# Optimization experiments

Measured on AMD Instinct MI355X. Metric: run time of the kernel, lower is better.

Reference implementation:

```python
import jax, jax.numpy as jnp
import numpy as np

H, DH, DIM = 8, 64, 512
GAMMA, LAMBDA_REG = 0.01, 0.001


def setup_inputs() -> dict:
    key = jax.random.key(0)
    ks = jax.random.split(key, 12)
    Q, N = 4, 1024
    f = lambda k, shape, s=0.02: jax.random.normal(k, shape, dtype=jnp.float32) * s
    return {
        "q": jax.random.normal(ks[0], (Q, N, DIM), dtype=jnp.float32),
        "k": jax.random.normal(ks[1], (Q, N, DIM), dtype=jnp.float32),
        "v": jax.random.normal(ks[2], (Q, N, DIM), dtype=jnp.float32),
        "ln_w": jnp.ones((DIM,), jnp.float32),
        "ln_b": jnp.zeros((DIM,), jnp.float32),
        "W_in": f(ks[3], (DIM, H * DH)),
        "W_out": f(ks[4], (H * DH, DIM)),
        "b_out": jnp.zeros((DIM,), jnp.float32),
        "wp_W1": f(ks[5], (2 * DH, 4 * DH), 0.05),
        "wp_b1": jnp.zeros((4 * DH,), jnp.float32),
        "wp_ln_w": jnp.ones((4 * DH,), jnp.float32),
        "wp_ln_b": jnp.zeros((4 * DH,), jnp.float32),
        "wp_W2": f(ks[6], (4 * DH, 3 * DH), 0.05),
        "wp_b2": jnp.zeros((3 * DH,), jnp.float32),
        "wp_W3": f(ks[7], (3 * DH, DH), 0.05),
        "wp_b3": jnp.zeros((DH,), jnp.float32),
        "wp_W4": f(ks[8], (DH, 3), 0.05),
        "wp_b4": jnp.zeros((3,), jnp.float32),
        "weight_temp": jnp.ones((1,), jnp.float32) * 0.1,
    }


def _layernorm(x, w, b, eps=1e-5):
    mu = x.mean(-1, keepdims=True)
    var = x.var(-1, keepdims=True)  # biased, matches torch LayerNorm
    return (x - mu) / jnp.sqrt(var + eps) * w + b


def reference(q, k, v, ln_w, ln_b, W_in, W_out, b_out,
              wp_W1, wp_b1, wp_ln_w, wp_ln_b, wp_W2, wp_b2,
              wp_W3, wp_b3, wp_W4, wp_b4, weight_temp):
    # input_linear: LN -> Linear(no bias) -> (dropout=identity in eval)
    def proj(t):
        x = _layernorm(t, ln_w, ln_b) @ W_in  # [Q, N, H*DH]
        Qn, Nn = x.shape[0], x.shape[1]
        return x.reshape(Qn, Nn, H, DH).transpose(2, 0, 1, 3)  # h q n d

    fq, fk, fv = proj(q), proj(k), proj(v)
    m = fk.shape[2]

    # --- cosine component (cosine_distance + extra clamp) ---
    raw = jnp.einsum('hqnd,hqmd->hqnm', fq, fk)
    n1 = jnp.linalg.norm(fq, axis=-1)[..., :, None] + 1e-6
    n2 = jnp.linalg.norm(fk, axis=-1)[..., None, :] + 1e-6
    cosine_sim = jnp.clip(raw / (n1 * n2), -0.95, 0.95)

    # --- regularized covariance component ---
    fkc = fk - fk.mean(axis=2, keepdims=True)       # center keys over token dim
    fqc = fq - fq.mean(axis=-1, keepdims=True)      # center queries over feature dim
    cov = jnp.einsum('hqnd,hqmd->hqnm', fqc, fkc) / (DH ** 0.5 + 1e-4)
    cov = jnp.clip((LAMBDA_REG / max(m, 1)) * cov, -50.0, 50.0)

    # --- margin-based variance component (eval: adaptive_gamma = gamma) ---
    fqn = fq / jnp.maximum(jnp.linalg.norm(fq, axis=-1, keepdims=True), 1e-4)
    fkn = fk / jnp.maximum(jnp.linalg.norm(fk, axis=-1, keepdims=True), 1e-4)
    cs = jnp.clip(jnp.einsum('hqnd,hqmd->hqnm', fqn, fkn), -0.95, 0.95)
    margin = jnp.clip(GAMMA - cs, 0.0, 15.0)
    var_comp = jnp.broadcast_to(margin.mean(-1, keepdims=True), cs.shape)

    # --- dynamic per-head weights via MLP predictor ---
    feat = jnp.concatenate([fq.mean(axis=(1, 2)), fk.mean(axis=(1, 2))], axis=-1)  # (h, 2*DH)
    h1 = jax.nn.relu(_layernorm(feat @ wp_W1 + wp_b1, wp_ln_w, wp_ln_b))
    h2 = jax.nn.relu(h1 @ wp_W2 + wp_b2)
    h3 = jax.nn.relu(h2 @ wp_W3 + wp_b3)
    probs = jax.nn.softmax(h3 @ wp_W4 + wp_b4, axis=-1)  # predictor ends in Softmax
    wt = jnp.clip(weight_temp, 0.01, 1.0)
    w = jax.nn.softmax(probs / wt, axis=-1)
    w = jnp.clip(w, 0.01, 0.95)
    w = w / w.sum(-1, keepdims=True)
    cos_w = w[:, 0].reshape(H, 1, 1, 1)
    cov_w = w[:, 1].reshape(H, 1, 1, 1)
    var_w = w[:, 2].reshape(H, 1, 1, 1)

    # --- std-normalized weighted combination (torch.std is unbiased, detached) ---
    sg = jax.lax.stop_gradient
    ustd = lambda x: jnp.std(x, ddof=1)
    dots = (cos_w * (cosine_sim / (sg(ustd(cosine_sim)) + 1e-4))
            + cov_w * (cov / (sg(ustd(cov)) + 1e-4) * 0.3)
            + var_w * (var_comp / (sg(ustd(var_comp)) + 1e-4) * 0.3))

    ds = ustd(dots)  # NOT detached in original
    temp = jnp.where(ds < 1e-5, 0.01, jnp.where(ds < 1e-3, 0.05, 0.2 + ds * 2.0))
    temp = jnp.clip(temp, 0.01, 8.0)

    attn = jax.nn.softmax(dots / temp, axis=-1)
    out = jnp.einsum('hqnm,hqmd->hqnd', attn, fv)
    out = out.transpose(1, 2, 0, 3).reshape(out.shape[1], out.shape[2], H * DH)  # q n (h d)
    return out @ W_out + b_out
```

## Files before the change

### kernel.cpp

```cpp
#include <hip/hip_runtime.h>
#include <math.h>

typedef _Float16 f16;
typedef _Float16 v8h __attribute__((ext_vector_type(8)));
typedef _Float16 v4h __attribute__((ext_vector_type(4)));
typedef float    v4f __attribute__((ext_vector_type(4)));

#define MFMA(a, b, c) __builtin_amdgcn_mfma_f32_16x16x32_f16((a), (b), (c), 0, 0, 0)

#define OFF_LN16    0u
#define OFF_FQ16    4194304u
#define OFF_FK16    5242880u
#define OFF_FVHT    6291456u
#define OFF_WINTH   8388608u
#define OFF_WOUTTH  8650752u
#define OFF_AVH     8912896u
#define OFF_AVL     9961472u
#define OFF_RQ1     11010048u
#define OFF_RQ2     11042816u
#define OFF_MUQ     11075584u
#define OFF_RK1     11108352u
#define OFF_RK2     11141120u
#define OFF_SK      11173888u
#define OFF_VC      11206656u
#define OFF_ROWCOS  11272192u
#define OFF_ROWCOV  11337728u
#define OFF_NUACC   11403264u
#define OFF_PB      11405312u
#define OFF_HS      11411456u
#define OFF_RP      11411520u
#define OFF_FEAT    11411712u
#define OFF_WV      11412736u
#define OFF_SCAL    11412760u

__device__ __forceinline__ float clampf(float x, float lo, float hi) {
    return fminf(fmaxf(x, lo), hi);
}

__global__ void k_zero(float* feat, float* nuacck) {
    int i = blockIdx.x * 256 + threadIdx.x;
    if (i < 1024) feat[i] = 0.0f;
    if (i < 2048) nuacck[i] = 0.0f;
}

__global__ __launch_bounds__(256) void k_wprep(const float* __restrict__ Win,
        const float* __restrict__ Wout, f16* __restrict__ WinTh,
        f16* __restrict__ WoutTh) {
    __shared__ float lds[64][68];
    const float* W = blockIdx.z ? Wout : Win;
    f16* Th = blockIdx.z ? WoutTh : WinTh;
    int k0 = blockIdx.y * 64, c0 = blockIdx.x * 64;
    int t = threadIdx.x;
    #pragma unroll
    for (int p = 0; p < 4; ++p) {
        int flat = p * 1024 + t * 4;
        int r = flat >> 6, c = flat & 63;
        *(float4*)&lds[r][c] = *(const float4*)&W[(size_t)(k0 + r) * 512 + c0 + c];
    }
    __syncthreads();
    int c = t >> 2, kk = (t & 3) * 16;
    #pragma unroll
    for (int half = 0; half < 2; ++half) {
        v8h h8;
        #pragma unroll
        for (int ii = 0; ii < 8; ++ii)
            h8[ii] = (f16)lds[kk + half * 8 + ii][c];
        *(v8h*)&Th[(size_t)(c0 + c) * 512 + k0 + kk + half * 8] = h8;
    }
}

__global__ __launch_bounds__(256) void k_ln16(const float* __restrict__ q,
        const float* __restrict__ kk, const float* __restrict__ v,
        const float* __restrict__ lnw, const float* __restrict__ lnb,
        f16* __restrict__ ln16) {
    int t = threadIdx.x, wid = t >> 6, lane = t & 63;
    int token = blockIdx.x * 4 + wid;
    int inp = token >> 12, lt = token & 4095;
    const float* xp = (inp == 0) ? q : ((inp == 1) ? kk : v);
    const float4* xr = (const float4*)(xp + (size_t)lt * 512);
    float4 a = xr[lane], b = xr[lane + 64];
    float s = a.x + a.y + a.z + a.w + b.x + b.y + b.z + b.w;
    float s2 = a.x*a.x + a.y*a.y + a.z*a.z + a.w*a.w
             + b.x*b.x + b.y*b.y + b.z*b.z + b.w*b.w;
    for (int o = 32; o > 0; o >>= 1) { s += __shfl_down(s, o); s2 += __shfl_down(s2, o); }
    float m_ = __shfl(s, 0) * (1.0f / 512.0f);
    float var = __shfl(s2, 0) * (1.0f / 512.0f) - m_ * m_;
    var = fmaxf(var, 0.0f);
    float rs = rsqrtf(var + 1e-5f);
    const float4* w4 = (const float4*)lnw;
    const float4* b4 = (const float4*)lnb;
    float4 wa = w4[lane], wb = w4[lane + 64], ba = b4[lane], bb = b4[lane + 64];
    f16* orow = ln16 + (size_t)token * 512;
    v4h ha, hb;
    ha[0] = (f16)((a.x - m_) * rs * wa.x + ba.x);
    ha[1] = (f16)((a.y - m_) * rs * wa.y + ba.y);
    ha[2] = (f16)((a.z - m_) * rs * wa.z + ba.z);
    ha[3] = (f16)((a.w - m_) * rs * wa.w + ba.w);
    hb[0] = (f16)((b.x - m_) * rs * wb.x + bb.x);
    hb[1] = (f16)((b.y - m_) * rs * wb.y + bb.y);
    hb[2] = (f16)((b.z - m_) * rs * wb.z + bb.z);
    hb[3] = (f16)((b.w - m_) * rs * wb.w + bb.w);
    *(v4h*)&orow[lane * 4] = ha;
    *(v4h*)&orow[lane * 4 + 256] = hb;
}

template<int MODE>
__device__ __forceinline__ void proj_body(const f16* __restrict__ A16,
        const f16* __restrict__ BTh,
        f16* __restrict__ fout16, f16* __restrict__ fhT,
        float* __restrict__ oA, float* __restrict__ oB, float* __restrict__ oC,
        float* __restrict__ feat, float* __restrict__ nuacck) {
    int t = threadIdx.x, l = t & 63, w = t >> 6;
    int wr = w >> 1, wc = w & 1;
    int col0 = blockIdx.x * 128 + wc * 64;
    int tok0 = blockIdx.y * 128 + wr * 64;
    int lr = l & 15, kg = (l >> 4) * 8;
    int rg4 = (l >> 4) * 4;
    v4f acc[4][4] = {};
    for (int ks = 0; ks < 512; ks += 32) {
        v8h a[4], b[4];
        #pragma unroll
        for (int i = 0; i < 4; ++i)
            a[i] = *(const v8h*)&A16[(size_t)(tok0 + i * 16 + lr) * 512 + ks + kg];
        #pragma unroll
        for (int j = 0; j < 4; ++j)
            b[j] = *(const v8h*)&BTh[(size_t)(col0 + j * 16 + lr) * 512 + ks + kg];
        #pragma unroll
        for (int i = 0; i < 4; ++i)
            #pragma unroll
            for (int j = 0; j < 4; ++j)
                acc[i][j] = MFMA(a[i], b[j], acc[i][j]);
    }
    int h = col0 >> 6;
    #pragma unroll
    for (int i = 0; i < 4; ++i)
        #pragma unroll
        for (int j = 0; j < 4; ++j)
            #pragma unroll
            for (int r = 0; r < 4; ++r) {
                int token = tok0 + i * 16 + rg4 + r;
                int d = j * 16 + lr;
                int qi = token >> 10, n = token & 1023;
                float val = acc[i][j][r];
                if constexpr (MODE != 2) {
                    fout16[((size_t)((h << 2) + qi) * 1024 + n) * 64 + d] = (f16)val;
                } else {
                    fhT[((size_t)((h << 2) + qi) * 64 + d) * 1024 + n] = (f16)val;
                }
            }
    if constexpr (MODE != 2) {
        #pragma unroll
        for (int i = 0; i < 4; ++i)
            #pragma unroll
            for (int r = 0; r < 4; ++r) {
                float s = 0.f, s2 = 0.f;
                #pragma unroll
                for (int j = 0; j < 4; ++j) { float v = acc[i][j][r]; s += v; s2 += v * v; }
                #pragma unroll
                for (int mk = 1; mk <= 8; mk <<= 1) {
                    s += __shfl_xor(s, mk); s2 += __shfl_xor(s2, mk);
                }
                if (lr == 0) {
                    int token = tok0 + i * 16 + rg4 + r;
                    int qi = token >> 10, n = token & 1023;
                    int row = ((h << 2) + qi) * 1024 + n;
                    float nv = sqrtf(s2);
                    oA[row] = 1.0f / (nv + 1e-6f);
                    oB[row] = 1.0f / fmaxf(nv, 1e-4f);
                    oC[row] = (MODE == 0) ? s * (1.0f / 64.0f) : s;
                }
            }
        float cs[4];
        #pragma unroll
        for (int j = 0; j < 4; ++j) {
            float c = 0.f;
            #pragma unroll
            for (int i = 0; i < 4; ++i)
                #pragma unroll
                for (int r = 0; r < 4; ++r) c += acc[i][j][r];
            c += __shfl_xor(c, 16); c += __shfl_xor(c, 32);
            cs[j] = c;
        }
        if (l < 16) {
            #pragma unroll
            for (int j = 0; j < 4; ++j)
                atomicAdd(&feat[h * 128 + (MODE == 1 ? 64 : 0) + j * 16 + l],
                          cs[j] * (1.0f / 4096.0f));
            if constexpr (MODE == 1) {
                int qi = tok0 >> 10;
                #pragma unroll
                for (int j = 0; j < 4; ++j)
                    atomicAdd(&nuacck[((h << 2) + qi) * 64 + j * 16 + l], cs[j]);
            }
        }
    }
}

__global__ __launch_bounds__(256) void k_proj_all(const f16* __restrict__ ln16,
        const f16* __restrict__ BTh,
        f16* __restrict__ fq16, f16* __restrict__ fk16,
        f16* __restrict__ fvhT,
        float* __restrict__ rq1, float* __restrict__ rq2, float* __restrict__ muq,
        float* __restrict__ rk1, float* __restrict__ rk2, float* __restrict__ sk,
        float* __restrict__ feat, float* __restrict__ nuacck) {
    int mode = blockIdx.z;
    if (mode == 0)
        proj_body<0>(ln16, BTh, fq16, nullptr, rq1, rq2, muq, feat, nullptr);
    else if (mode == 1)
        proj_body<1>(ln16 + 2097152u, BTh, fk16, nullptr, rk1, rk2, sk, feat, nuacck);
    else
        proj_body<2>(ln16 + 4194304u, BTh, nullptr, fvhT,
                     nullptr, nullptr, nullptr, nullptr, nullptr);
}

__global__ __launch_bounds__(256) void k_mlp(const float* __restrict__ feat,
        const float* __restrict__ W1, const float* __restrict__ b1,
        const float* __restrict__ lw, const float* __restrict__ lb,
        const float* __restrict__ W2, const float* __restrict__ b2,
        const float* __restrict__ W3, const float* __restrict__ b3,
        const float* __restrict__ W4, const float* __restrict__ b4,
        const float* __restrict__ wtemp, float* wv) {
    __shared__ float h1[256], h2[192], h3[64], red[8];
    int t = threadIdx.x;
    int h = blockIdx.x;
    float p = 0.0f;
    for (int i = 0; i < 128; ++i) p += feat[h * 128 + i] * W1[i * 256 + t];
    p += b1[t];
    float s = p, s2 = p * p;
    for (int o = 32; o > 0; o >>= 1) { s += __shfl_down(s, o); s2 += __shfl_down(s2, o); }
    if ((t & 63) == 0) { red[t >> 6] = s; red[4 + (t >> 6)] = s2; }
    __syncthreads();
    float S = red[0] + red[1] + red[2] + red[3];
    float S2 = red[4] + red[5] + red[6] + red[7];
    float mu = S / 256.0f;
    float var = S2 / 256.0f - mu * mu; if (var < 0.0f) var = 0.0f;
    float xh = (p - mu) * rsqrtf(var + 1e-5f) * lw[t] + lb[t];
    h1[t] = fmaxf(xh, 0.0f);
    __syncthreads();
    if (t < 192) {
        float a = 0.0f;
        for (int i = 0; i < 256; ++i) a += h1[i] * W2[i * 192 + t];
        h2[t] = fmaxf(a + b2[t], 0.0f);
    }
    __syncthreads();
    if (t < 64) {
        float a = 0.0f;
        for (int i = 0; i < 192; ++i) a += h2[i] * W3[i * 64 + t];
        h3[t] = fmaxf(a + b3[t], 0.0f);
    }
    __syncthreads();
    if (t == 0) {
        float lg[3];
        for (int j = 0; j < 3; ++j) {
            float a = 0.0f;
            for (int i = 0; i < 64; ++i) a += h3[i] * W4[i * 3 + j];
            lg[j] = a + b4[j];
        }
        float mx = fmaxf(lg[0], fmaxf(lg[1], lg[2]));
        float e0 = expf(lg[0] - mx), e1 = expf(lg[1] - mx), e2 = expf(lg[2] - mx);
        float se = e0 + e1 + e2;
        float pr0 = e0 / se, pr1 = e1 / se, pr2 = e2 / se;
        float wt = wtemp[0]; wt = fminf(fmaxf(wt, 0.01f), 1.0f);
        float q0 = pr0 / wt, q1 = pr1 / wt, q2 = pr2 / wt;
        float m2 = fmaxf(q0, fmaxf(q1, q2));
        float f0 = expf(q0 - m2), f1 = expf(q1 - m2), f2 = expf(q2 - m2);
        float sf = f0 + f1 + f2; f0 /= sf; f1 /= sf; f2 /= sf;
        f0 = fminf(fmaxf(f0, 0.01f), 0.95f);
        f1 = fminf(fmaxf(f1, 0.01f), 0.95f);
        f2 = fminf(fmaxf(f2, 0.01f), 0.95f);
        float sw = f0 + f1 + f2;
        wv[h * 3 + 0] = f0 / sw; wv[h * 3 + 1] = f1 / sw; wv[h * 3 + 2] = f2 / sw;
    }
}

#define PASS_PREAMBLE_AB                                                       \
    int hq = blockIdx.z;                                                       \
    int half = blockIdx.y;                                                     \
    int m0base = half * 512;                                                   \
    int t = threadIdx.x, l = t & 63, w = t >> 6;                               \
    int lr = l & 15, kg = (l >> 4) * 8, rg4 = (l >> 4) * 4;                    \
    int nb = blockIdx.x * 64 + w * 16;                                         \
    const f16* Q = fq16 + (size_t)hq * 65536;                                  \
    const f16* K = fk16 + (size_t)hq * 65536;                                  \
    v8h aq0 = *(const v8h*)&Q[(size_t)(nb + lr) * 64 + kg];                    \
    v8h aq1 = *(const v8h*)&Q[(size_t)(nb + lr) * 64 + 32 + kg];               \
    const float inv1024 = 1.0f / 1024.0f;                                      \
    float uvp = nuacck[hq * 64 + l] * inv1024;                                 \
    _Pragma("unroll")                                                          \
    for (int o = 32; o > 0; o >>= 1) uvp += __shfl_xor(uvp, o);                \
    float uv = uvp;                                                            \
    float tp = 0.f;                                                            \
    _Pragma("unroll")                                                          \
    for (int e = 0; e < 8; ++e)                                                \
        tp += (float)aq0[e] * nuacck[hq * 64 + kg + e]                         \
            + (float)aq1[e] * nuacck[hq * 64 + 32 + kg + e];                   \
    tp *= inv1024;                                                             \
    tp += __shfl_xor(tp, 16);                                                  \
    tp += __shfl_xor(tp, 32);                                                  \
    float muv[4], tv[4];                                                       \
    _Pragma("unroll")                                                          \
    for (int r = 0; r < 4; ++r) {                                              \
        muv[r] = muq[hq * 1024 + nb + rg4 + r];                                \
        tv[r] = __shfl(tp, rg4 + r);                                           \
    }                                                                          \
    const float Acs = (0.001f / 1024.0f) / 8.0001f;                            \
    float Pr[4], Gr[4];                                                        \
    _Pragma("unroll")                                                          \
    for (int r = 0; r < 4; ++r) {                                              \
        Gr[r] = Acs * muv[r];                                                  \
        Pr[r] = Acs * fmaf(muv[r], uv, -tv[r]);                                \
    }

#define LOAD_KTILE(m0a)                                                        \
    v8h b0[4], b1[4];                                                          \
    _Pragma("unroll")                                                          \
    for (int j = 0; j < 4; ++j) {                                              \
        b0[j] = *(const v8h*)&K[(size_t)((m0a) + j * 16 + lr) * 64 + kg];      \
        b1[j] = *(const v8h*)&K[(size_t)((m0a) + j * 16 + lr) * 64 + 32 + kg]; \
    }

__global__ __launch_bounds__(256) void k_passA(const f16* __restrict__ fq16,
        const f16* __restrict__ fk16, const float* __restrict__ rq1,
        const float* __restrict__ rq2, const float* __restrict__ muq,
        const float* __restrict__ rk1, const float* __restrict__ rk2,
        const float* __restrict__ sk, const float* __restrict__ nuacck,
        float* __restrict__ vcrow, float* __restrict__ rowcos,
        float* __restrict__ rowcov, float* __restrict__ pb) {
    __shared__ float rk1s[512], rk2s[512], sks[512];
    PASS_PREAMBLE_AB
    {
        int i2 = t * 2;
        *(float2*)&rk1s[i2] = *(const float2*)&rk1[hq * 1024 + m0base + i2];
        *(float2*)&rk2s[i2] = *(const float2*)&rk2[hq * 1024 + m0base + i2];
        *(float2*)&sks[i2]  = *(const float2*)&sk[hq * 1024 + m0base + i2];
    }
    __syncthreads();
    float rq1v[4], rq2v[4];
    #pragma unroll
    for (int r = 0; r < 4; ++r) {
        rq1v[r] = rq1[hq * 1024 + nb + rg4 + r];
        rq2v[r] = rq2[hq * 1024 + nb + rg4 + r];
    }
    float scos = 0, s2cos = 0, scov = 0, s2cov = 0, sccov = 0;
    float mp[4] = {}, rcs[4] = {}, rcv[4] = {};
    #pragma unroll 2
    for (int m0 = 0; m0 < 512; m0 += 64) {
        LOAD_KTILE(m0base + m0)
        float rk1v[4], rk2v[4], skv[4];
        #pragma unroll
        for (int j = 0; j < 4; ++j) {
            int cg = m0 + j * 16 + lr;
            rk1v[j] = rk1s[cg]; rk2v[j] = rk2s[cg]; skv[j] = sks[cg];
        }
        v4f acc[4] = {};
        #pragma unroll
        for (int j = 0; j < 4; ++j) {
            acc[j] = MFMA(aq0, b0[j], acc[j]);
            acc[j] = MFMA(aq1, b1[j], acc[j]);
        }
        #pragma unroll
        for (int j = 0; j < 4; ++j)
            #pragma unroll
            for (int r = 0; r < 4; ++r) {
                float rv = acc[j][r];
                float cosv = clampf(rv * rq1v[r] * rk1v[j], -0.95f, 0.95f);
                float x2 = rv * rq2v[r] * rk2v[j];
                float marg = fmaxf(0.01f - fmaxf(x2, -0.95f), 0.0f);
                float cov = fmaf(-Gr[r], skv[j], fmaf(Acs, rv, Pr[r]));
                scos += cosv; s2cos = fmaf(cosv, cosv, s2cos);
                scov += cov;  s2cov = fmaf(cov, cov, s2cov);
                sccov = fmaf(cosv, cov, sccov);
                mp[r] += marg; rcs[r] += cosv; rcv[r] += cov;
            }
    }
    #pragma unroll
    for (int r = 0; r < 4; ++r) {
        float m_ = mp[r], c_ = rcs[r], v_ = rcv[r];
        #pragma unroll
        for (int mk = 1; mk <= 8; mk <<= 1) {
            m_ += __shfl_xor(m_, mk);
            c_ += __shfl_xor(c_, mk);
            v_ += __shfl_xor(v_, mk);
        }
        if (lr == 0) {
            int row = hq * 1024 + nb + rg4 + r;
            vcrow[half * 32768 + row] = m_ * inv1024;
            rowcos[half * 32768 + row] = c_;
            rowcov[half * 32768 + row] = v_;
        }
    }
    for (int o = 32; o > 0; o >>= 1) {
        scos += __shfl_down(scos, o); s2cos += __shfl_down(s2cos, o);
        scov += __shfl_down(scov, o); s2cov += __shfl_down(s2cov, o);
        sccov += __shfl_down(sccov, o);
    }
    __shared__ float bs[4][5];
    if (l == 0) { bs[w][0] = scos; bs[w][1] = s2cos; bs[w][2] = scov;
                  bs[w][3] = s2cov; bs[w][4] = sccov; }
    __syncthreads();
    if (t == 0) {
        int bid = (hq * 2 + half) * 16 + blockIdx.x;
        #pragma unroll
        for (int s = 0; s < 5; ++s)
            pb[bid * 6 + s] = bs[0][s] + bs[1][s] + bs[2][s] + bs[3][s];
    }
}

__global__ __launch_bounds__(256) void k_fin1(const float* __restrict__ pb,
        const float* __restrict__ vcrow, float* __restrict__ hs,
        float* __restrict__ scal) {
    __shared__ float hsl[40];
    int t = threadIdx.x;
    int hd = t >> 5, idx = t & 31;
    double a0 = 0, a1 = 0, a2 = 0, a3 = 0, a4 = 0;
    for (int i = idx; i < 128; i += 32) {
        const float* p = &pb[(hd * 128 + i) * 6];
        a0 += p[0]; a1 += p[1]; a2 += p[2]; a3 += p[3]; a4 += p[4];
    }
    for (int m = 1; m <= 16; m <<= 1) {
        a0 += __shfl_xor(a0, m); a1 += __shfl_xor(a1, m); a2 += __shfl_xor(a2, m);
        a3 += __shfl_xor(a3, m); a4 += __shfl_xor(a4, m);
    }
    if (idx == 0) {
        hsl[hd * 5 + 0] = (float)a0; hsl[hd * 5 + 1] = (float)a1;
        hsl[hd * 5 + 2] = (float)a2; hsl[hd * 5 + 3] = (float)a3;
        hsl[hd * 5 + 4] = (float)a4;
        hs[hd * 5 + 0] = (float)a0; hs[hd * 5 + 1] = (float)a1;
        hs[hd * 5 + 2] = (float)a2; hs[hd * 5 + 3] = (float)a3;
        hs[hd * 5 + 4] = (float)a4;
    }
    double s4 = 0, s5 = 0;
    for (int i = t; i < 32768; i += 256) {
        double rm = (double)(vcrow[i] + vcrow[32768 + i]);
        s4 += rm; s5 += rm * rm;
    }
    for (int o = 32; o > 0; o >>= 1) { s4 += __shfl_down(s4, o); s5 += __shfl_down(s5, o); }
    __shared__ double red[2][4];
    int wid = t >> 6, lane = t & 63;
    if (lane == 0) { red[0][wid] = s4; red[1][wid] = s5; }
    __syncthreads();
    if (t == 0) {
        double S4 = red[0][0] + red[0][1] + red[0][2] + red[0][3];
        double S5 = red[1][0] + red[1][1] + red[1][2] + red[1][3];
        double S0 = 0, S1 = 0, S2 = 0, S3 = 0;
        for (int h2 = 0; h2 < 8; ++h2) {
            S0 += hsl[h2 * 5 + 0]; S1 += hsl[h2 * 5 + 1];
            S2 += hsl[h2 * 5 + 2]; S3 += hsl[h2 * 5 + 3];
        }
        const double cnt = 33554432.0;
        scal[0] = (float)sqrt(fmax(0.0, (S1 - S0 * S0 / cnt) / (cnt - 1.0)));
        scal[1] = (float)sqrt(fmax(0.0, (S3 - S2 * S2 / cnt) / (cnt - 1.0)));
        double V4 = S4 * 1024.0, V5 = S5 * 1024.0;
        scal[2] = (float)sqrt(fmax(0.0, (V5 - V4 * V4 / cnt) / (cnt - 1.0)));
    }
}

__global__ __launch_bounds__(256) void k_finrow(const float* __restrict__ vcrow,
        const float* __restrict__ rowcos, const float* __restrict__ rowcov,
        const float* __restrict__ wv, const float* __restrict__ scal,
        float* __restrict__ rp) {
    int t = threadIdx.x;
    float s1 = scal[0] + 1e-4f, s2v = scal[1] + 1e-4f, s3 = scal[2] + 1e-4f;
    float p1 = 0, p2 = 0, p3 = 0;
    #pragma unroll
    for (int i = 0; i < 2; ++i) {
        int row = blockIdx.x * 512 + i * 256 + t;
        int h = row >> 12;
        float fc1 = wv[h * 3] / s1;
        float fc2 = wv[h * 3 + 1] * 0.3f / s2v;
        float c3 = wv[h * 3 + 2] * 0.3f / s3;
        float a = (vcrow[row] + vcrow[32768 + row]) * c3;
        float b = fc1 * (rowcos[row] + rowcos[32768 + row])
                + fc2 * (rowcov[row] + rowcov[32768 + row]);
        p1 += a; p2 = fmaf(a, a, p2); p3 = fmaf(a, b, p3);
    }
    for (int o = 32; o > 0; o >>= 1) {
        p1 += __shfl_down(p1, o); p2 += __shfl_down(p2, o); p3 += __shfl_down(p3, o);
    }
    __shared__ float red[3][4];
    int wid = t >> 6, lane = t & 63;
    if (lane == 0) { red[0][wid] = p1; red[1][wid] = p2; red[2][wid] = p3; }
    __syncthreads();
    if (t == 0) {
        rp[blockIdx.x * 3 + 0] = red[0][0] + red[0][1] + red[0][2] + red[0][3];
        rp[blockIdx.x * 3 + 1] = red[1][0] + red[1][1] + red[1][2] + red[1][3];
        rp[blockIdx.x * 3 + 2] = red[2][0] + red[2][1] + red[2][2] + red[2][3];
    }
}

__global__ __launch_bounds__(64) void k_fin2(const float* __restrict__ rp,
        const float* __restrict__ hs, const float* __restrict__ wv,
        float* __restrict__ scal) {
    int t = threadIdx.x;
    double p1 = rp[t * 3 + 0], p2 = rp[t * 3 + 1], p3 = rp[t * 3 + 2];
    for (int o = 32; o > 0; o >>= 1) {
        p1 += __shfl_down(p1, o); p2 += __shfl_down(p2, o); p3 += __shfl_down(p3, o);
    }
    if (t == 0) {
        double s1 = (double)scal[0] + 1e-4, s2v = (double)scal[1] + 1e-4;
        double sdd = 1024.0 * p1;
        double sdd2 = 2.0 * p3 + 1024.0 * p2;
        for (int h = 0; h < 8; ++h) {
            double fc1 = (double)wv[h * 3] / s1;
            double fc2 = (double)wv[h * 3 + 1] * 0.3 / s2v;
            sdd += fc1 * hs[h * 5 + 0] + fc2 * hs[h * 5 + 2];
            sdd2 += fc1 * fc1 * hs[h * 5 + 1] + fc2 * fc2 * hs[h * 5 + 3]
                  + 2.0 * fc1 * fc2 * hs[h * 5 + 4];
        }
        const double cnt = 33554432.0;
        double ds = sqrt(fmax(0.0, (sdd2 - sdd * sdd / cnt) / (cnt - 1.0)));
        float temp = (ds < 1e-5) ? 0.01f : ((ds < 1e-3) ? 0.05f : (0.2f + (float)ds * 2.0f));
        temp = fminf(fmaxf(temp, 0.01f), 8.0f);
        scal[3] = temp;
    }
}

#define TILE_STEP(PBASE, MK)                                                   \
    {                                                                          \
        int mk = (MK);                                                         \
        v8h b0[4], b1[4];                                                      \
        _Pragma("unroll")                                                      \
        for (int j = 0; j < 4; ++j) {                                          \
            b0[j] = *(const v8h*)&K[(size_t)(mk + j * 16 + lr) * 64 + kg];     \
            b1[j] = *(const v8h*)&K[(size_t)(mk + j * 16 + lr) * 64 + 32 + kg];\
        }                                                                      \
        float rk1v[4], skv[4];                                                 \
        _Pragma("unroll")                                                      \
        for (int j = 0; j < 4; ++j) {                                          \
            int cg = mk + j * 16 + lr;                                         \
            rk1v[j] = rk1s[cg]; skv[j] = sks[cg];                              \
        }                                                                      \
        v4f acc[4] = {};                                                       \
        _Pragma("unroll")                                                      \
        for (int j = 0; j < 4; ++j) {                                          \
            acc[j] = MFMA(aq0, b0[j], acc[j]);                                 \
            acc[j] = MFMA(aq1, b1[j], acc[j]);                                 \
        }                                                                      \
        float dd[4][4];                                                        \
        float tmax[4] = { -1e30f, -1e30f, -1e30f, -1e30f };                    \
        _Pragma("unroll")                                                      \
        for (int j = 0; j < 4; ++j)                                            \
            _Pragma("unroll")                                                  \
            for (int r = 0; r < 4; ++r) {                                      \
                float rv = acc[j][r];                                          \
                float cosv = clampf(rv * rq1v[r] * rk1v[j], -0.95f, 0.95f);    \
                float cov = fmaf(-Gcr[r], skv[j], fmaf(Acs, rv, Pcr[r]));      \
                float d2 = fmaf(fc2, cov, fmaf(fc1, cosv, addc[r]));           \
                dd[j][r] = d2;                                                 \
                tmax[r] = fmaxf(tmax[r], d2);                                  \
            }                                                                  \
        v4f fv;                                                                \
        _Pragma("unroll")                                                      \
        for (int r = 0; r < 4; ++r) {                                          \
            float tm = tmax[r];                                                \
            tm = fmaxf(tm, __shfl_xor(tm, 1));                                 \
            tm = fmaxf(tm, __shfl_xor(tm, 2));                                 \
            tm = fmaxf(tm, __shfl_xor(tm, 4));                                 \
            tm = fmaxf(tm, __shfl_xor(tm, 8));                                 \
            float mnew = fmaxf(mrun[r], tm);                                   \
            float fr_ = __expf((mrun[r] - mnew) * invt);                       \
            mrun[r] = mnew;                                                    \
            rsacc[r] *= fr_;                                                   \
            fv[r] = fr_;                                                       \
        }                                                                      \
        _Pragma("unroll")                                                      \
        for (int j = 0; j < 4; ++j) accpv[j] *= fv;                            \
        _Pragma("unroll")                                                      \
        for (int j = 0; j < 4; ++j)                                            \
            _Pragma("unroll")                                                  \
            for (int r = 0; r < 4; ++r) {                                      \
                float pe = __expf((dd[j][r] - mrun[r]) * invt);                \
                f16 p16 = (f16)pe;                                             \
                rsacc[r] += (float)p16;                                        \
                (PBASE)[(w * 16 + rg4 + r) * 72 + j * 16 + lr] = p16;          \
            }                                                                  \
        v8h pa0 = *(const v8h*)&(PBASE)[(w * 16 + lr) * 72 + kg];              \
        v8h pa1 = *(const v8h*)&(PBASE)[(w * 16 + lr) * 72 + 32 + kg];         \
        _Pragma("unroll")                                                      \
        for (int j = 0; j < 4; ++j) {                                          \
            size_t vb = ((size_t)hq * 64 + j * 16 + lr) * 1024 + mk;           \
            v8h vh0 = *(const v8h*)&fvhT[vb + kg];                             \
            v8h vh1 = *(const v8h*)&fvhT[vb + 32 + kg];                        \
            accpv[j] = MFMA(pa0, vh0, accpv[j]);                               \
            accpv[j] = MFMA(pa1, vh1, accpv[j]);                               \
        }                                                                      \
    }

__global__ __launch_bounds__(512) void k_passC(const f16* __restrict__ fq16,
        const f16* __restrict__ fk16, const float* __restrict__ rq1,
        const float* __restrict__ muq, const float* __restrict__ rk1,
        const float* __restrict__ sk, const float* __restrict__ nuacck,
        const float* __restrict__ vcrow, const float* __restrict__ wv,
        const float* __restrict__ scal,
        const f16* __restrict__ fvhT,
        f16* __restrict__ avh, f16* __restrict__ avl) {
    __shared__ __align__(16) char arena[36864];
    __shared__ float rk1s[1024], sks[1024];
    f16* Pa = (f16*)arena;
    f16* Pb = (f16*)(arena + 18432);
    int hq = blockIdx.y;
    int t = threadIdx.x, l = t & 63, w = t >> 6;
    int rg = w & 3, kh = w >> 2;
    int lr = l & 15, kg = (l >> 4) * 8, rg4 = (l >> 4) * 4;
    int nb = blockIdx.x * 64 + rg * 16;
    int m0base = kh * 512;
    const f16* Q = fq16 + (size_t)hq * 65536;
    const f16* K = fk16 + (size_t)hq * 65536;
    {
        int i2 = t * 2;
        *(float2*)&rk1s[i2] = *(const float2*)&rk1[hq * 1024 + i2];
        *(float2*)&sks[i2]  = *(const float2*)&sk[hq * 1024 + i2];
    }
    __syncthreads();
    v8h aq0 = *(const v8h*)&Q[(size_t)(nb + lr) * 64 + kg];
    v8h aq1 = *(const v8h*)&Q[(size_t)(nb + lr) * 64 + 32 + kg];
    const float inv1024 = 1.0f / 1024.0f;
    float uvp = nuacck[hq * 64 + l] * inv1024;
    #pragma unroll
    for (int o = 32; o > 0; o >>= 1) uvp += __shfl_xor(uvp, o);
    float uv = uvp;
    float tpv = 0.f;
    #pragma unroll
    for (int e = 0; e < 8; ++e)
        tpv += (float)aq0[e] * nuacck[hq * 64 + kg + e]
             + (float)aq1[e] * nuacck[hq * 64 + 32 + kg + e];
    tpv *= inv1024;
    tpv += __shfl_xor(tpv, 16);
    tpv += __shfl_xor(tpv, 32);
    float muv[4], tv[4];
    #pragma unroll
    for (int r = 0; r < 4; ++r) {
        muv[r] = muq[hq * 1024 + nb + rg4 + r];
        tv[r] = __shfl(tpv, rg4 + r);
    }
    const float Acs = (0.001f / 1024.0f) / 8.0001f;
    float Pcr[4], Gcr[4];
    #pragma unroll
    for (int r = 0; r < 4; ++r) {
        Gcr[r] = Acs * muv[r];
        Pcr[r] = Acs * fmaf(muv[r], uv, -tv[r]);
    }
    int h = hq >> 2;
    float s1 = scal[0] + 1e-4f, s2v = scal[1] + 1e-4f, s3 = scal[2] + 1e-4f;
    float fc1 = wv[h * 3] / s1;
    float fc2 = wv[h * 3 + 1] * 0.3f / s2v;
    float c3 = wv[h * 3 + 2] * 0.3f / s3;
    float invt = 1.0f / scal[3];
    float rq1v[4], addc[4];
    #pragma unroll
    for (int r = 0; r < 4; ++r) {
        int row = hq * 1024 + nb + rg4 + r;
        rq1v[r] = rq1[row];
        addc[r] = (vcrow[row] + vcrow[32768 + row]) * c3;
    }
    v4f accpv[4] = {};
    float rsacc[4] = {};
    float mrun[4] = { -1e30f, -1e30f, -1e30f, -1e30f };
    for (int it = 0; it < 4; ++it) {
        TILE_STEP(Pa, m0base + it * 128)
        TILE_STEP(Pb, m0base + it * 128 + 64)
    }
    __syncthreads();
    #pragma unroll
    for (int r = 0; r < 4; ++r) {
        float s = rsacc[r];
        s += __shfl_xor(s, 1); s += __shfl_xor(s, 2);
        s += __shfl_xor(s, 4); s += __shfl_xor(s, 8);
        rsacc[r] = s;
    }
    float* cbacc = (float*)arena;
    float* cbrs  = (float*)(arena + 16384);
    float* cbm   = (float*)(arena + 20480);
    if (kh == 1) {
        #pragma unroll
        for (int j = 0; j < 4; ++j)
            #pragma unroll
            for (int r = 0; r < 4; ++r)
                cbacc[(rg * 16 + j * 4 + r) * 64 + l] = accpv[j][r];
        #pragma unroll
        for (int r = 0; r < 4; ++r) cbrs[(rg * 4 + r) * 64 + l] = rsacc[r];
        if (lr == 0) {
            #pragma unroll
            for (int r = 0; r < 4; ++r) cbm[rg * 16 + rg4 + r] = mrun[r];
        }
    }
    __syncthreads();
    if (kh == 0) {
        v4f f0v, f1v;
        float rinv[4];
        #pragma unroll
        for (int r = 0; r < 4; ++r) {
            float m1 = cbm[rg * 16 + rg4 + r];
            float mf = fmaxf(mrun[r], m1);
            float f0 = __expf((mrun[r] - mf) * invt);
            float f1 = __expf((m1 - mf) * invt);
            f0v[r] = f0; f1v[r] = f1;
            float rst = rsacc[r] * f0 + cbrs[(rg * 4 + r) * 64 + l] * f1;
            rinv[r] = 1.0f / rst;
        }
        #pragma unroll
        for (int j = 0; j < 4; ++j)
            #pragma unroll
            for (int r = 0; r < 4; ++r) {
                float val = (accpv[j][r] * f0v[r]
                           + cbacc[(rg * 16 + j * 4 + r) * 64 + l] * f1v[r]) * rinv[r];
                size_t idx = ((size_t)(hq * 1024 + nb + rg4 + r)) * 64 + j * 16 + lr;
                f16 hi = (f16)val;
                avh[idx] = hi;
                avl[idx] = (f16)(val - (float)hi);
            }
    }
}

__global__ __launch_bounds__(256) void k_out_mfma(const f16* __restrict__ avh,
        const f16* __restrict__ avl,
        const f16* __restrict__ WoutTh,
        const float* __restrict__ bout, float* __restrict__ out) {
    __shared__ float red[2][4][4][4][64];
    int t = threadIdx.x, l = t & 63, w = t >> 6;
    int wc = w & 1, kh = w >> 1;
    int col0 = blockIdx.x * 128 + wc * 64;
    int tok0 = blockIdx.y * 64;
    int qi = tok0 >> 10, nb = tok0 & 1023;
    int lr = l & 15, kg = (l >> 4) * 8;
    v4f acc[4][4] = {};
    for (int ks8 = 0; ks8 < 8; ++ks8) {
        int ks = kh * 256 + ks8 * 32;
        int f = ks + kg;
        int h = f >> 6, d = f & 63;
        size_t hb = (size_t)((h << 2) + qi) * 1024;
        v8h ah[4], al4[4], bh[4];
        #pragma unroll
        for (int i = 0; i < 4; ++i) {
            int n = nb + i * 16 + lr;
            ah[i]  = *(const v8h*)&avh[(hb + n) * 64 + d];
            al4[i] = *(const v8h*)&avl[(hb + n) * 64 + d];
        }
        #pragma unroll
        for (int j = 0; j < 4; ++j)
            bh[j] = *(const v8h*)&WoutTh[(size_t)(col0 + j * 16 + lr) * 512 + ks + kg];
        #pragma unroll
        for (int i = 0; i < 4; ++i)
            #pragma unroll
            for (int j = 0; j < 4; ++j) {
                acc[i][j] = MFMA(ah[i], bh[j], acc[i][j]);
                acc[i][j] = MFMA(al4[i], bh[j], acc[i][j]);
            }
    }
    if (kh == 0) {
        #pragma unroll
        for (int i = 0; i < 4; ++i)
            #pragma unroll
            for (int j = 0; j < 4; ++j)
                #pragma unroll
                for (int r = 0; r < 4; ++r)
                    red[wc][i][j][r][l] = acc[i][j][r];
    }
    __syncthreads();
    if (kh == 1) {
        #pragma unroll
        for (int i = 0; i < 4; ++i)
            #pragma unroll
            for (int j = 0; j < 4; ++j) {
                int col = col0 + j * 16 + lr;
                float bo = bout[col];
                #pragma unroll
                for (int r = 0; r < 4; ++r) {
                    float val = acc[i][j][r] + red[wc][i][j][r][l] + bo;
                    int token = tok0 + i * 16 + (l >> 4) * 4 + r;
                    out[(size_t)token * 512 + col] = val;
                }
            }
    }
}

extern "C" void kernel_launch(void* const* d_in, const int* in_sizes, int n_in,
                              void* d_out, int out_size, void* d_ws, size_t ws_size,
                              hipStream_t stream) {
    const float* q     = (const float*)d_in[0];
    const float* k     = (const float*)d_in[1];
    const float* v     = (const float*)d_in[2];
    const float* ln_w  = (const float*)d_in[3];
    const float* ln_b  = (const float*)d_in[4];
    const float* W_in  = (const float*)d_in[5];
    const float* W_out = (const float*)d_in[6];
    const float* b_out = (const float*)d_in[7];
    const float* wp_W1 = (const float*)d_in[8];
    const float* wp_b1 = (const float*)d_in[9];
    const float* wp_lw = (const float*)d_in[10];
    const float* wp_lb = (const float*)d_in[11];
    const float* wp_W2 = (const float*)d_in[12];
    const float* wp_b2 = (const float*)d_in[13];
    const float* wp_W3 = (const float*)d_in[14];
    const float* wp_b3 = (const float*)d_in[15];
    const float* wp_W4 = (const float*)d_in[16];
    const float* wp_b4 = (const float*)d_in[17];
    const float* wtemp = (const float*)d_in[18];

    float* ws = (float*)d_ws;
    f16* ln16     = (f16*)(ws + OFF_LN16);
    f16* fq16     = (f16*)(ws + OFF_FQ16);
    f16* fk16     = (f16*)(ws + OFF_FK16);
    f16* fvhT     = (f16*)(ws + OFF_FVHT);
    f16* WinTh    = (f16*)(ws + OFF_WINTH);
    f16* WoutTh   = (f16*)(ws + OFF_WOUTTH);
    f16* avh      = (f16*)(ws + OFF_AVH);
    f16* avl      = (f16*)(ws + OFF_AVL);
    float* rq1    = ws + OFF_RQ1;
    float* rq2    = ws + OFF_RQ2;
    float* muq    = ws + OFF_MUQ;
    float* rk1    = ws + OFF_RK1;
    float* rk2    = ws + OFF_RK2;
    float* sk     = ws + OFF_SK;
    float* vcrow  = ws + OFF_VC;
    float* rowcos = ws + OFF_ROWCOS;
    float* rowcov = ws + OFF_ROWCOV;
    float* nuacck = ws + OFF_NUACC;
    float* pb     = ws + OFF_PB;
    float* hs     = ws + OFF_HS;
    float* rp     = ws + OFF_RP;
    float* feat   = ws + OFF_FEAT;
    float* wv     = ws + OFF_WV;
    float* scal   = ws + OFF_SCAL;

    k_zero<<<8, 256, 0, stream>>>(feat, nuacck);
    k_wprep<<<dim3(8, 8, 2), 256, 0, stream>>>(W_in, W_out, WinTh, WoutTh);
    k_ln16<<<3072, 256, 0, stream>>>(q, k, v, ln_w, ln_b, ln16);
    k_proj_all<<<dim3(4, 32, 3), 256, 0, stream>>>(ln16, WinTh,
            fq16, fk16, fvhT, rq1, rq2, muq, rk1, rk2, sk, feat, nuacck);
    k_mlp<<<8, 256, 0, stream>>>(feat, wp_W1, wp_b1, wp_lw, wp_lb,
                                 wp_W2, wp_b2, wp_W3, wp_b3, wp_W4, wp_b4,
                                 wtemp, wv);
    k_passA<<<dim3(16, 2, 32), 256, 0, stream>>>(fq16, fk16, rq1, rq2, muq, rk1, rk2,
                                                 sk, nuacck, vcrow, rowcos, rowcov, pb);
    k_fin1<<<1, 256, 0, stream>>>(pb, vcrow, hs, scal);
    k_finrow<<<64, 256, 0, stream>>>(vcrow, rowcos, rowcov, wv, scal, rp);
    k_fin2<<<1, 64, 0, stream>>>(rp, hs, wv, scal);
    k_passC<<<dim3(16, 32), 512, 0, stream>>>(fq16, fk16, rq1, muq, rk1, sk, nuacck,
                                              vcrow, wv, scal, fvhT, avh, avl);
    k_out_mfma<<<dim3(4, 64), 256, 0, stream>>>(avh, avl, WoutTh, b_out,
                                                (float*)d_out);
}
```

Baseline: 262.1 us.

## Precompute per-row softmax max bound in passA to drop online rescaling in passC

passA now also records, for each row, the maximum clamped cosine and covariance values, reduced across lanes and written for both halves. passC combines these with its positive weights into an upper bound on each row's logit maximum. Each tile then exponentiates directly against that fixed bound. This removes the per-tile max reduction, the running-max exp rescaling of the accumulators, and the final cross-wave max merge. The trade-off is a few extra writes and reads, and a bound that can be looser than the true max, which risks underflow or precision loss in the f16 probabilities if the cosine and covariance maxima land on different columns.

```diff
diff --git a/kernel.cpp b/kernel.cpp
--- a/kernel.cpp
+++ b/kernel.cpp
@@ -32,6 +32,8 @@
 #define OFF_FEAT    11411712u
 #define OFF_WV      11412736u
 #define OFF_SCAL    11412760u
+#define OFF_MAXC    11412768u
+#define OFF_MAXV    11478304u
 
 __device__ __forceinline__ float clampf(float x, float lo, float hi) {
     return fminf(fmaxf(x, lo), hi);
@@ -325,7 +327,8 @@
         const float* __restrict__ rk1, const float* __restrict__ rk2,
         const float* __restrict__ sk, const float* __restrict__ nuacck,
         float* __restrict__ vcrow, float* __restrict__ rowcos,
-        float* __restrict__ rowcov, float* __restrict__ pb) {
+        float* __restrict__ rowcov, float* __restrict__ maxc,
+        float* __restrict__ maxv, float* __restrict__ pb) {
     __shared__ float rk1s[512], rk2s[512], sks[512];
     PASS_PREAMBLE_AB
     {
@@ -343,6 +346,8 @@
     }
     float scos = 0, s2cos = 0, scov = 0, s2cov = 0, sccov = 0;
     float mp[4] = {}, rcs[4] = {}, rcv[4] = {};
+    float mcs[4] = { -1e30f, -1e30f, -1e30f, -1e30f };
+    float mcv[4] = { -1e30f, -1e30f, -1e30f, -1e30f };
     #pragma unroll 2
     for (int m0 = 0; m0 < 512; m0 += 64) {
         LOAD_KTILE(m0base + m0)
@@ -371,22 +376,29 @@
                 scov += cov;  s2cov = fmaf(cov, cov, s2cov);
                 sccov = fmaf(cosv, cov, sccov);
                 mp[r] += marg; rcs[r] += cosv; rcv[r] += cov;
+                mcs[r] = fmaxf(mcs[r], cosv);
+                mcv[r] = fmaxf(mcv[r], cov);
             }
     }
     #pragma unroll
     for (int r = 0; r < 4; ++r) {
         float m_ = mp[r], c_ = rcs[r], v_ = rcv[r];
+        float xc = mcs[r], xv = mcv[r];
         #pragma unroll
         for (int mk = 1; mk <= 8; mk <<= 1) {
             m_ += __shfl_xor(m_, mk);
             c_ += __shfl_xor(c_, mk);
             v_ += __shfl_xor(v_, mk);
+            xc = fmaxf(xc, __shfl_xor(xc, mk));
+            xv = fmaxf(xv, __shfl_xor(xv, mk));
         }
         if (lr == 0) {
             int row = hq * 1024 + nb + rg4 + r;
             vcrow[half * 32768 + row] = m_ * inv1024;
             rowcos[half * 32768 + row] = c_;
             rowcov[half * 32768 + row] = v_;
+            maxc[half * 32768 + row] = xc;
+            maxv[half * 32768 + row] = xv;
         }
     }
     for (int o = 32; o > 0; o >>= 1) {
@@ -536,8 +548,6 @@
             acc[j] = MFMA(aq0, b0[j], acc[j]);                                 \
             acc[j] = MFMA(aq1, b1[j], acc[j]);                                 \
         }                                                                      \
-        float dd[4][4];                                                        \
-        float tmax[4] = { -1e30f, -1e30f, -1e30f, -1e30f };                    \
         _Pragma("unroll")                                                      \
         for (int j = 0; j < 4; ++j)                                            \
             _Pragma("unroll")                                                  \
@@ -546,30 +556,7 @@
                 float cosv = clampf(rv * rq1v[r] * rk1v[j], -0.95f, 0.95f);    \
                 float cov = fmaf(-Gcr[r], skv[j], fmaf(Acs, rv, Pcr[r]));      \
                 float d2 = fmaf(fc2, cov, fmaf(fc1, cosv, addc[r]));           \
-                dd[j][r] = d2;                                                 \
-                tmax[r] = fmaxf(tmax[r], d2);                                  \
-            }                                                                  \
-        v4f fv;                                                                \
-        _Pragma("unroll")                                                      \
-        for (int r = 0; r < 4; ++r) {                                          \
-            float tm = tmax[r];                                                \
-            tm = fmaxf(tm, __shfl_xor(tm, 1));                                 \
-            tm = fmaxf(tm, __shfl_xor(tm, 2));                                 \
-            tm = fmaxf(tm, __shfl_xor(tm, 4));                                 \
-            tm = fmaxf(tm, __shfl_xor(tm, 8));                                 \
-            float mnew = fmaxf(mrun[r], tm);                                   \
-            float fr_ = __expf((mrun[r] - mnew) * invt);                       \
-            mrun[r] = mnew;                                                    \
-            rsacc[r] *= fr_;                                                   \
-            fv[r] = fr_;                                                       \
-        }                                                                      \
-        _Pragma("unroll")                                                      \
-        for (int j = 0; j < 4; ++j) accpv[j] *= fv;                            \
-        _Pragma("unroll")                                                      \
-        for (int j = 0; j < 4; ++j)                                            \
-            _Pragma("unroll")                                                  \
-            for (int r = 0; r < 4; ++r) {                                      \
-                float pe = __expf((dd[j][r] - mrun[r]) * invt);                \
+                float pe = __expf(fmaf(d2, invt, -mxr[r]));                    \
                 f16 p16 = (f16)pe;                                             \
                 rsacc[r] += (float)p16;                                        \
                 (PBASE)[(w * 16 + rg4 + r) * 72 + j * 16 + lr] = p16;          \
@@ -590,7 +577,8 @@
         const f16* __restrict__ fk16, const float* __restrict__ rq1,
         const float* __restrict__ muq, const float* __restrict__ rk1,
         const float* __restrict__ sk, const float* __restrict__ nuacck,
-        const float* __restrict__ vcrow, const float* __restrict__ wv,
+        const float* __restrict__ vcrow, const float* __restrict__ maxca,
+        const float* __restrict__ maxva, const float* __restrict__ wv,
         const float* __restrict__ scal,
         const f16* __restrict__ fvhT,
         f16* __restrict__ avh, f16* __restrict__ avl) {
@@ -646,16 +634,18 @@
     float fc2 = wv[h * 3 + 1] * 0.3f / s2v;
     float c3 = wv[h * 3 + 2] * 0.3f / s3;
     float invt = 1.0f / scal[3];
-    float rq1v[4], addc[4];
+    float rq1v[4], addc[4], mxr[4];
     #pragma unroll
     for (int r = 0; r < 4; ++r) {
         int row = hq * 1024 + nb + rg4 + r;
         rq1v[r] = rq1[row];
         addc[r] = (vcrow[row] + vcrow[32768 + row]) * c3;
+        float mc = fmaxf(maxca[row], maxca[32768 + row]);
+        float mv = fmaxf(maxva[row], maxva[32768 + row]);
+        mxr[r] = fmaf(fc1, mc, fmaf(fc2, mv, addc[r])) * invt;
     }
     v4f accpv[4] = {};
     float rsacc[4] = {};
-    float mrun[4] = { -1e30f, -1e30f, -1e30f, -1e30f };
     for (int it = 0; it < 4; ++it) {
         TILE_STEP(Pa, m0base + it * 128)
         TILE_STEP(Pb, m0base + it * 128 + 64)
@@ -670,7 +660,6 @@
     }
     float* cbacc = (float*)arena;
     float* cbrs  = (float*)(arena + 16384);
-    float* cbm   = (float*)(arena + 20480);
     if (kh == 1) {
         #pragma unroll
         for (int j = 0; j < 4; ++j)
@@ -679,31 +668,19 @@
                 cbacc[(rg * 16 + j * 4 + r) * 64 + l] = accpv[j][r];
         #pragma unroll
         for (int r = 0; r < 4; ++r) cbrs[(rg * 4 + r) * 64 + l] = rsacc[r];
-        if (lr == 0) {
-            #pragma unroll
-            for (int r = 0; r < 4; ++r) cbm[rg * 16 + rg4 + r] = mrun[r];
-        }
     }
     __syncthreads();
     if (kh == 0) {
-        v4f f0v, f1v;
         float rinv[4];
         #pragma unroll
-        for (int r = 0; r < 4; ++r) {
-            float m1 = cbm[rg * 16 + rg4 + r];
-            float mf = fmaxf(mrun[r], m1);
-            float f0 = __expf((mrun[r] - mf) * invt);
-            float f1 = __expf((m1 - mf) * invt);
-            f0v[r] = f0; f1v[r] = f1;
-            float rst = rsacc[r] * f0 + cbrs[(rg * 4 + r) * 64 + l] * f1;
-            rinv[r] = 1.0f / rst;
-        }
+        for (int r = 0; r < 4; ++r)
+            rinv[r] = 1.0f / (rsacc[r] + cbrs[(rg * 4 + r) * 64 + l]);
         #pragma unroll
         for (int j = 0; j < 4; ++j)
             #pragma unroll
             for (int r = 0; r < 4; ++r) {
-                float val = (accpv[j][r] * f0v[r]
-                           + cbacc[(rg * 16 + j * 4 + r) * 64 + l] * f1v[r]) * rinv[r];
+                float val = (accpv[j][r] + cbacc[(rg * 16 + j * 4 + r) * 64 + l])
+                            * rinv[r];
                 size_t idx = ((size_t)(hq * 1024 + nb + rg4 + r)) * 64 + j * 16 + lr;
                 f16 hi = (f16)val;
                 avh[idx] = hi;
@@ -815,6 +792,8 @@
     float* vcrow  = ws + OFF_VC;
     float* rowcos = ws + OFF_ROWCOS;
     float* rowcov = ws + OFF_ROWCOV;
+    float* maxc   = ws + OFF_MAXC;
+    float* maxv   = ws + OFF_MAXV;
     float* nuacck = ws + OFF_NUACC;
     float* pb     = ws + OFF_PB;
     float* hs     = ws + OFF_HS;
@@ -832,12 +811,14 @@
                                  wp_W2, wp_b2, wp_W3, wp_b3, wp_W4, wp_b4,
                                  wtemp, wv);
     k_passA<<<dim3(16, 2, 32), 256, 0, stream>>>(fq16, fk16, rq1, rq2, muq, rk1, rk2,
-                                                 sk, nuacck, vcrow, rowcos, rowcov, pb);
+                                                 sk, nuacck, vcrow, rowcos, rowcov,
+                                                 maxc, maxv, pb);
     k_fin1<<<1, 256, 0, stream>>>(pb, vcrow, hs, scal);
     k_finrow<<<64, 256, 0, stream>>>(vcrow, rowcos, rowcov, wv, scal, rp);
     k_fin2<<<1, 64, 0, stream>>>(rp, hs, wv, scal);
     k_passC<<<dim3(16, 32), 512, 0, stream>>>(fq16, fk16, rq1, muq, rk1, sk, nuacck,
-                                              vcrow, wv, scal, fvhT, avh, avl);
+                                              vcrow, maxc, maxv, wv, scal,
+                                              fvhT, avh, avl);
     k_out_mfma<<<dim3(4, 64), 256, 0, stream>>>(avh, avl, WoutTh, b_out,
                                                 (float*)d_out);
 }
```

Result: faster. 248.7 us (-5.1%).
